# Kernel optimization log

Measured on AMD Instinct MI355X. Metric: run time of the kernel, lower is better.

Reference implementation:

```python
import jax, jax.numpy as jnp
import numpy as np

NUM_EMBEDDINGS = 1024
EMBEDDING_DIM = 256


def setup_inputs() -> dict:
    key = jax.random.key(0)
    kx, kw = jax.random.split(key)
    x = jax.random.normal(kx, (64, 32, 32, EMBEDDING_DIM), dtype=jnp.float32)
    # nn.Embedding default init: N(0, 1)
    embedding_weight = jax.random.normal(kw, (NUM_EMBEDDINGS, EMBEDDING_DIM), dtype=jnp.float32)
    return {"x": x, "embedding_weight": embedding_weight}


def reference(x, embedding_weight):
    D = embedding_weight.shape[1]
    x_flat = x.reshape(-1, D)  # [N, D]
    distances = (
        jnp.sum(x_flat * x_flat, axis=1, keepdims=True)
        + jnp.sum(embedding_weight * embedding_weight, axis=1)
        - 2.0 * jnp.matmul(x_flat, embedding_weight.T)
    )
    indices = jnp.argmin(distances, axis=1)  # [N]
    quantized = embedding_weight[indices].reshape(x.shape)
    return quantized, indices
```

## Files before the change

kernel.cpp:

```cpp
#include <hip/hip_runtime.h>


#define K_EMB  1024
#define D_DIM  256
#define N_ROWS 65536

typedef unsigned int u32;
typedef unsigned long long u64;
typedef __attribute__((ext_vector_type(8)))  _Float16 f16x8;
typedef __attribute__((ext_vector_type(4)))  _Float16 f16x4;
typedef __attribute__((ext_vector_type(16))) float    f32x16;

__device__ __forceinline__ u32 f32_sortable(float f) {
    u32 u = __float_as_uint(f);
    return u ^ ((u32)((int)u >> 31) | 0x80000000u);
}
__device__ __forceinline__ float f32_unsort(u32 u) {
    u32 v = (u & 0x80000000u) ? (u ^ 0x80000000u) : ~u;
    return __uint_as_float(v);
}

#define GLDS(gp, lp) __builtin_amdgcn_global_load_lds( \
    (const __attribute__((address_space(1))) void*)(gp), \
    (__attribute__((address_space(3))) void*)(lp), 16, 0, 0)

__global__ void vq_prep(const float* __restrict__ emb,
                        _Float16* __restrict__ ehi,
                        _Float16* __restrict__ cn2,
                        float* __restrict__ cnormf) {
    int gid = blockIdx.x * 256 + threadIdx.x;
    int code = gid >> 6, lane = gid & 63;
    float4 v = ((const float4*)(emb + (size_t)code * D_DIM))[lane];
    f16x4 hv = {(_Float16)v.x, (_Float16)v.y, (_Float16)v.z, (_Float16)v.w};
    ((f16x4*)(ehi + (size_t)code * D_DIM))[lane] = hv;
    float s = v.x * v.x + v.y * v.y + v.z * v.z + v.w * v.w;
    #pragma unroll
    for (int off = 32; off > 0; off >>= 1) s += __shfl_down(s, off, 64);
    if (lane == 0) {
        float cn = 0.5f * s;
        cnormf[code] = cn;
        _Float16 ch = (_Float16)cn;
        _Float16 cl = (_Float16)(cn - (float)ch);
        f16x8 e = {};
        e[0] = (_Float16)(-(float)ch);
        e[1] = (_Float16)(-(float)cl);
        ((f16x8*)cn2)[code] = e;
    }
}

__global__ __launch_bounds__(256, 2) void vq_main(
    const float* __restrict__ x, const float* __restrict__ emb,
    const _Float16* __restrict__ eh, const _Float16* __restrict__ cn2,
    const float* __restrict__ cnormf,
    float* __restrict__ outq, float* __restrict__ outi)
{
    __shared__ _Float16 Ab[2][2048 * 8];
    __shared__ int winners[128];

    const int t = threadIdx.x, w = t >> 6, lane = t & 63;
    const int m = lane & 31, kh = lane >> 5;
    const int rowbase = blockIdx.x * 128 + w * 32;
    const int myrow = rowbase + m;
    const int kh4 = kh * 4;

    f16x8 bh[16];
    {
        const float* xr = x + (size_t)myrow * D_DIM + kh * 8;
        #pragma unroll
        for (int s = 0; s < 16; s++) {
            float4 v0 = *(const float4*)(xr + s * 16);
            float4 v1 = *(const float4*)(xr + s * 16 + 4);
            f16x8 h = {(_Float16)v0.x, (_Float16)v0.y, (_Float16)v0.z, (_Float16)v0.w,
                       (_Float16)v1.x, (_Float16)v1.y, (_Float16)v1.z, (_Float16)v1.w};
            bh[s] = h;
        }
    }
    f16x8 xe = {};
    if (kh == 0) { xe[0] = (_Float16)1.0f; xe[1] = (_Float16)1.0f; }

    u32 b1 = 0, b2 = 0, b3 = 0;

    auto stage = [&](int c) {
        _Float16* dst = &Ab[c & 1][0];
        const _Float16* src = eh + (size_t)(c * 64 + lane) * D_DIM + w * 64;
        #pragma unroll
        for (int i = 0; i < 8; i++)
            GLDS(src + i * 8, dst + (w * 8 + i) * 512);
    };
    auto compute = [&](int buf, f32x16& a0, f32x16& a1, int c) {
        const f16x8* Af = (const f16x8*)&Ab[buf][0];
        f16x8 e0 = ((const f16x8*)cn2)[c * 64 + m];
        f16x8 e1 = ((const f16x8*)cn2)[c * 64 + 32 + m];
        a0 = (f32x16){}; a1 = (f32x16){};
        #pragma unroll
        for (int s = 0; s < 16; s++) {
            f16x8 fa0 = Af[m      + 64 * (2 * s + kh)];
            f16x8 fa1 = Af[32 + m + 64 * (2 * s + kh)];
            a0 = __builtin_amdgcn_mfma_f32_32x32x16_f16(fa0, bh[s], a0, 0, 0, 0);
            a1 = __builtin_amdgcn_mfma_f32_32x32x16_f16(fa1, bh[s], a1, 0, 0, 0);
        }
        a0 = __builtin_amdgcn_mfma_f32_32x32x16_f16(e0, xe, a0, 0, 0, 0);
        a1 = __builtin_amdgcn_mfma_f32_32x32x16_f16(e1, xe, a1, 0, 0, 0);
    };
    auto top3ins = [&](u32 p) {
        u32 t2 = b1 < p ? b1 : p;
        u32 t3 = b2 < p ? b2 : p;
        b1 = b1 > p ? b1 : p;
        b2 = t2 > b2 ? t2 : b2;
        b3 = t3 > b3 ? t3 : b3;
    };
    auto top3p = [&](const f32x16& a0, const f32x16& a1, int c) {
        const u32 sbase = (u32)(c * 64) + kh4;
        #pragma unroll
        for (int tt = 0; tt < 2; tt++) {
            #pragma unroll
            for (int r = 0; r < 16; r++) {
                float sc = tt ? a1[r] : a0[r];
                u32 code = sbase + tt * 32 + (r & 3) + 8 * (r >> 2);
                u32 p = (f32_sortable(sc) & 0xFFFFFC00u) | code;
                top3ins(p);
            }
        }
    };

    f32x16 accA0, accA1, accB0, accB1;
    stage(0);
    for (int cc = 0; cc < 16; cc += 2) {
        __syncthreads();
        if (cc + 1 < 16) stage(cc + 1);
        compute(0, accA0, accA1, cc);
        if (cc) top3p(accB0, accB1, cc - 1);
        __syncthreads();
        if (cc + 2 < 16) stage(cc + 2);
        compute(1, accB0, accB1, cc + 1);
        top3p(accA0, accA1, cc);
    }
    top3p(accB0, accB1, 15);

    {
        u32 p1 = (u32)__shfl_xor((int)b1, 32, 64);
        u32 p2 = (u32)__shfl_xor((int)b2, 32, 64);
        u32 p3 = (u32)__shfl_xor((int)b3, 32, 64);
        top3ins(p1); top3ins(p2); top3ins(p3);
    }

    float s1f = f32_unsort(b1), s2f = f32_unsort(b2), s3f = f32_unsort(b3);
    u32 i1 = b1 & 1023u, i2 = b2 & 1023u, i3 = b3 & 1023u;
    bool need = (s1f - s2f) <= 0.25f;
    if (kh == 0 && !need) winners[w * 32 + m] = (int)i1;
    u64 mask = __ballot(kh == 0 && need);
    while (mask) {
        int r = __ffsll((unsigned long long)mask) - 1;
        mask &= mask - 1;
        int row = rowbase + r;
        u32 c1 = (u32)__shfl((int)i1, r, 64);
        u32 c2 = (u32)__shfl((int)i2, r, 64);
        u32 c3 = (u32)__shfl((int)i3, r, 64);
        float g3 = __shfl(s1f - s3f, r, 64);
        int ncand = (g3 <= 0.25f) ? 3 : 2;
        float4 xv = ((const float4*)(x + (size_t)row * D_DIM))[lane];
        float bs = -3.0e38f; int bi = 0x7fffffff;
        u32 cand[3] = {c1, c2, c3};
        for (int q = 0; q < ncand; q++) {
            int ccd = (int)cand[q];
            float4 ev = ((const float4*)(emb + (size_t)ccd * D_DIM))[lane];
            float d = xv.x * ev.x + xv.y * ev.y + xv.z * ev.z + xv.w * ev.w;
            #pragma unroll
            for (int dd = 1; dd < 64; dd <<= 1) d += __shfl_xor(d, dd, 64);
            float sc = d - cnormf[ccd];
            if (sc > bs || (sc == bs && ccd < bi)) { bs = sc; bi = ccd; }
        }
        if (lane == 0) winners[w * 32 + r] = bi;
    }

    for (int r = 0; r < 32; r++) {
        int idx = winners[w * 32 + r];
        int row = rowbase + r;
        float4 qv = ((const float4*)(emb + (size_t)idx * D_DIM))[lane];
        ((float4*)(outq + (size_t)row * D_DIM))[lane] = qv;
    }
    if (kh == 0) outi[rowbase + m] = (float)winners[w * 32 + m];
}

extern "C" void kernel_launch(void* const* d_in, const int* in_sizes, int n_in,
                              void* d_out, int out_size, void* d_ws, size_t ws_size,
                              hipStream_t stream) {
    const float* x   = (const float*)d_in[0];
    const float* emb = (const float*)d_in[1];
    float* outq = (float*)d_out;
    float* outi = outq + (size_t)N_ROWS * D_DIM;

    _Float16* ehi = (_Float16*)d_ws;
    _Float16* cn2 = ehi + (size_t)K_EMB * D_DIM;
    float* cnormf = (float*)(cn2 + (size_t)K_EMB * 8);

    vq_prep<<<K_EMB / 4, 256, 0, stream>>>(emb, ehi, cn2, cnormf);
    vq_main<<<N_ROWS / 128, 256, 0, stream>>>(x, emb, ehi, cn2, cnormf,
                                              outq, outi);
}
```

Before: 166.4 us.

## Split codebook across wave pairs with 64-row register tiles and LDS top-3 merge

```diff
diff --git a/kernel.cpp b/kernel.cpp
--- a/kernel.cpp
+++ b/kernel.cpp
@@ -54,113 +54,140 @@
     const float* __restrict__ cnormf,
     float* __restrict__ outq, float* __restrict__ outi)
 {
-    __shared__ _Float16 Ab[2][2048 * 8];
+    __shared__ _Float16 T[2][2][8192];
+    __shared__ u32 xchg[2][128][3];
     __shared__ int winners[128];
 
     const int t = threadIdx.x, w = t >> 6, lane = t & 63;
     const int m = lane & 31, kh = lane >> 5;
-    const int rowbase = blockIdx.x * 128 + w * 32;
-    const int myrow = rowbase + m;
+    const int p = w >> 1;
+    const int h = w & 1;
+    const int blkrow = blockIdx.x * 128;
+    const int rowA = blkrow + p * 64 + m;
     const int kh4 = kh * 4;
 
-    f16x8 bh[16];
+    f16x8 bhA[16], bhB[16];
     {
-        const float* xr = x + (size_t)myrow * D_DIM + kh * 8;
+        const float* xr = x + (size_t)rowA * D_DIM + kh * 8;
         #pragma unroll
         for (int s = 0; s < 16; s++) {
             float4 v0 = *(const float4*)(xr + s * 16);
             float4 v1 = *(const float4*)(xr + s * 16 + 4);
-            f16x8 h = {(_Float16)v0.x, (_Float16)v0.y, (_Float16)v0.z, (_Float16)v0.w,
-                       (_Float16)v1.x, (_Float16)v1.y, (_Float16)v1.z, (_Float16)v1.w};
-            bh[s] = h;
+            bhA[s] = (f16x8){(_Float16)v0.x, (_Float16)v0.y, (_Float16)v0.z, (_Float16)v0.w,
+                             (_Float16)v1.x, (_Float16)v1.y, (_Float16)v1.z, (_Float16)v1.w};
+            float4 u0 = *(const float4*)(xr + 32 * D_DIM + s * 16);
+            float4 u1 = *(const float4*)(xr + 32 * D_DIM + s * 16 + 4);
+            bhB[s] = (f16x8){(_Float16)u0.x, (_Float16)u0.y, (_Float16)u0.z, (_Float16)u0.w,
+                             (_Float16)u1.x, (_Float16)u1.y, (_Float16)u1.z, (_Float16)u1.w};
         }
     }
     f16x8 xe = {};
     if (kh == 0) { xe[0] = (_Float16)1.0f; xe[1] = (_Float16)1.0f; }
 
-    u32 b1 = 0, b2 = 0, b3 = 0;
+    u32 A1 = 0, A2 = 0, A3 = 0, B1 = 0, B2 = 0, B3 = 0;
+
+    auto t3 = [](u32& c1, u32& c2, u32& c3, u32 pv) {
+        u32 u2 = c1 < pv ? c1 : pv;
+        u32 u3 = c2 < pv ? c2 : pv;
+        c1 = c1 > pv ? c1 : pv;
+        c2 = u2 > c2 ? u2 : c2;
+        c3 = u3 > c3 ? u3 : c3;
+    };
 
     auto stage = [&](int c) {
-        _Float16* dst = &Ab[c & 1][0];
-        const _Float16* src = eh + (size_t)(c * 64 + lane) * D_DIM + w * 64;
-        #pragma unroll
-        for (int i = 0; i < 8; i++)
-            GLDS(src + i * 8, dst + (w * 8 + i) * 512);
-    };
+        const int buf = c & 1;
+        #pragma unroll
+        for (int hh = 0; hh < 2; hh++) {
+            const _Float16* srcb = eh + (size_t)(hh * 512 + c * 32 + m) * D_DIM + (lane >> 5) * 8;
+            _Float16* dstb = &T[buf][hh][0];
+            #pragma unroll
+            for (int i = 0; i < 4; i++) {
+                int r = w * 4 + i;
+                GLDS(srcb + r * 16, dstb + r * 512);
+            }
+        }
+    };
+
     auto compute = [&](int buf, f32x16& a0, f32x16& a1, int c) {
-        const f16x8* Af = (const f16x8*)&Ab[buf][0];
-        f16x8 e0 = ((const f16x8*)cn2)[c * 64 + m];
-        f16x8 e1 = ((const f16x8*)cn2)[c * 64 + 32 + m];
+        const f16x8* Af = (const f16x8*)&T[buf][h][0];
+        f16x8 e = ((const f16x8*)cn2)[h * 512 + c * 32 + m];
         a0 = (f32x16){}; a1 = (f32x16){};
         #pragma unroll
         for (int s = 0; s < 16; s++) {
-            f16x8 fa0 = Af[m      + 64 * (2 * s + kh)];
-            f16x8 fa1 = Af[32 + m + 64 * (2 * s + kh)];
-            a0 = __builtin_amdgcn_mfma_f32_32x32x16_f16(fa0, bh[s], a0, 0, 0, 0);
-            a1 = __builtin_amdgcn_mfma_f32_32x32x16_f16(fa1, bh[s], a1, 0, 0, 0);
-        }
-        a0 = __builtin_amdgcn_mfma_f32_32x32x16_f16(e0, xe, a0, 0, 0, 0);
-        a1 = __builtin_amdgcn_mfma_f32_32x32x16_f16(e1, xe, a1, 0, 0, 0);
-    };
-    auto top3ins = [&](u32 p) {
-        u32 t2 = b1 < p ? b1 : p;
-        u32 t3 = b2 < p ? b2 : p;
-        b1 = b1 > p ? b1 : p;
-        b2 = t2 > b2 ? t2 : b2;
-        b3 = t3 > b3 ? t3 : b3;
-    };
+            f16x8 fa = Af[(2 * s + kh) * 32 + m];
+            a0 = __builtin_amdgcn_mfma_f32_32x32x16_f16(fa, bhA[s], a0, 0, 0, 0);
+            a1 = __builtin_amdgcn_mfma_f32_32x32x16_f16(fa, bhB[s], a1, 0, 0, 0);
+        }
+        a0 = __builtin_amdgcn_mfma_f32_32x32x16_f16(e, xe, a0, 0, 0, 0);
+        a1 = __builtin_amdgcn_mfma_f32_32x32x16_f16(e, xe, a1, 0, 0, 0);
+    };
+
     auto top3p = [&](const f32x16& a0, const f32x16& a1, int c) {
-        const u32 sbase = (u32)(c * 64) + kh4;
-        #pragma unroll
-        for (int tt = 0; tt < 2; tt++) {
-            #pragma unroll
-            for (int r = 0; r < 16; r++) {
-                float sc = tt ? a1[r] : a0[r];
-                u32 code = sbase + tt * 32 + (r & 3) + 8 * (r >> 2);
-                u32 p = (f32_sortable(sc) & 0xFFFFFC00u) | code;
-                top3ins(p);
-            }
-        }
-    };
-
-    f32x16 accA0, accA1, accB0, accB1;
+        const u32 sbase = (u32)(h * 512 + c * 32) + kh4;
+        #pragma unroll
+        for (int r = 0; r < 16; r++) {
+            u32 code = sbase + (r & 3) + 8 * (r >> 2);
+            u32 pa = (f32_sortable(a0[r]) & 0xFFFFFC00u) | code;
+            t3(A1, A2, A3, pa);
+            u32 pb = (f32_sortable(a1[r]) & 0xFFFFFC00u) | code;
+            t3(B1, B2, B3, pb);
+        }
+    };
+
+    f32x16 aA0, aA1, aB0, aB1;
     stage(0);
     for (int cc = 0; cc < 16; cc += 2) {
         __syncthreads();
         if (cc + 1 < 16) stage(cc + 1);
-        compute(0, accA0, accA1, cc);
-        if (cc) top3p(accB0, accB1, cc - 1);
+        compute(0, aA0, aA1, cc);
+        if (cc) top3p(aB0, aB1, cc - 1);
         __syncthreads();
         if (cc + 2 < 16) stage(cc + 2);
-        compute(1, accB0, accB1, cc + 1);
-        top3p(accA0, accA1, cc);
-    }
-    top3p(accB0, accB1, 15);
+        compute(1, aB0, aB1, cc + 1);
+        top3p(aA0, aA1, cc);
+    }
+    top3p(aB0, aB1, 15);
 
     {
-        u32 p1 = (u32)__shfl_xor((int)b1, 32, 64);
-        u32 p2 = (u32)__shfl_xor((int)b2, 32, 64);
-        u32 p3 = (u32)__shfl_xor((int)b3, 32, 64);
-        top3ins(p1); top3ins(p2); top3ins(p3);
-    }
-
-    float s1f = f32_unsort(b1), s2f = f32_unsort(b2), s3f = f32_unsort(b3);
-    u32 i1 = b1 & 1023u, i2 = b2 & 1023u, i3 = b3 & 1023u;
+        u32 q1 = (u32)__shfl_xor((int)A1, 32, 64);
+        u32 q2 = (u32)__shfl_xor((int)A2, 32, 64);
+        u32 q3 = (u32)__shfl_xor((int)A3, 32, 64);
+        t3(A1, A2, A3, q1); t3(A1, A2, A3, q2); t3(A1, A2, A3, q3);
+        q1 = (u32)__shfl_xor((int)B1, 32, 64);
+        q2 = (u32)__shfl_xor((int)B2, 32, 64);
+        q3 = (u32)__shfl_xor((int)B3, 32, 64);
+        t3(B1, B2, B3, q1); t3(B1, B2, B3, q2); t3(B1, B2, B3, q3);
+    }
+
+    if (kh == 0) {
+        int ra = p * 64 + m;
+        xchg[h][ra][0] = A1; xchg[h][ra][1] = A2; xchg[h][ra][2] = A3;
+        xchg[h][ra + 32][0] = B1; xchg[h][ra + 32][1] = B2; xchg[h][ra + 32][2] = B3;
+    }
+    __syncthreads();
+
+    const int rl = p * 64 + h * 32 + m;
+    u32 c1 = 0, c2 = 0, c3 = 0;
+    t3(c1, c2, c3, xchg[0][rl][0]); t3(c1, c2, c3, xchg[0][rl][1]); t3(c1, c2, c3, xchg[0][rl][2]);
+    t3(c1, c2, c3, xchg[1][rl][0]); t3(c1, c2, c3, xchg[1][rl][1]); t3(c1, c2, c3, xchg[1][rl][2]);
+
+    float s1f = f32_unsort(c1), s2f = f32_unsort(c2), s3f = f32_unsort(c3);
+    u32 i1 = c1 & 1023u, i2 = c2 & 1023u, i3 = c3 & 1023u;
     bool need = (s1f - s2f) <= 0.25f;
-    if (kh == 0 && !need) winners[w * 32 + m] = (int)i1;
+    if (kh == 0 && !need) winners[rl] = (int)i1;
     u64 mask = __ballot(kh == 0 && need);
     while (mask) {
         int r = __ffsll((unsigned long long)mask) - 1;
         mask &= mask - 1;
-        int row = rowbase + r;
-        u32 c1 = (u32)__shfl((int)i1, r, 64);
-        u32 c2 = (u32)__shfl((int)i2, r, 64);
-        u32 c3 = (u32)__shfl((int)i3, r, 64);
+        int row = blkrow + p * 64 + h * 32 + r;
+        u32 d1 = (u32)__shfl((int)i1, r, 64);
+        u32 d2 = (u32)__shfl((int)i2, r, 64);
+        u32 d3 = (u32)__shfl((int)i3, r, 64);
         float g3 = __shfl(s1f - s3f, r, 64);
         int ncand = (g3 <= 0.25f) ? 3 : 2;
         float4 xv = ((const float4*)(x + (size_t)row * D_DIM))[lane];
         float bs = -3.0e38f; int bi = 0x7fffffff;
-        u32 cand[3] = {c1, c2, c3};
+        u32 cand[3] = {d1, d2, d3};
         for (int q = 0; q < ncand; q++) {
             int ccd = (int)cand[q];
             float4 ev = ((const float4*)(emb + (size_t)ccd * D_DIM))[lane];
@@ -170,16 +197,18 @@
             float sc = d - cnormf[ccd];
             if (sc > bs || (sc == bs && ccd < bi)) { bs = sc; bi = ccd; }
         }
-        if (lane == 0) winners[w * 32 + r] = bi;
-    }
-
+        if (lane == 0) winners[p * 64 + h * 32 + r] = bi;
+    }
+
+    if (kh == 0) outi[blkrow + rl] = (float)winners[rl];
+    const int gbase = p * 64 + h * 32;
+    #pragma unroll 8
     for (int r = 0; r < 32; r++) {
-        int idx = winners[w * 32 + r];
-        int row = rowbase + r;
+        int idx = winners[gbase + r];
+        int row = blkrow + gbase + r;
         float4 qv = ((const float4*)(emb + (size_t)idx * D_DIM))[lane];
         ((float4*)(outq + (size_t)row * D_DIM))[lane] = qv;
     }
-    if (kh == 0) outi[rowbase + m] = (float)winners[w * 32 + m];
 }
 
 extern "C" void kernel_launch(void* const* d_in, const int* in_sizes, int n_in,
```

Measured after the change: 165.8 us. No clear change (-0.4%).
